# Optimization experiments

Measured on AMD Instinct MI355X. Metric: run time of the kernel, lower is better.

Reference implementation:

```python
import jax, jax.numpy as jnp
import numpy as np

N = 30000          # nodes
DEG = 16           # in-degree per node
E = N * DEG        # edges per etype
T = 3              # edge types
IN = 128           # in_feats
HID = 256          # hidden_size
HEADS = 4
CLS = 2            # num_classes
NEG_SLOPE = 0.2    # DGL GATConv default


def setup_inputs() -> dict:
    key = jax.random.key(0)
    ks = jax.random.split(key, 14)
    s = lambda k, shape: (jax.random.normal(k, shape, jnp.float32) * 0.05)
    feat = jax.random.normal(ks[0], (N, IN), jnp.float32)
    src = jax.random.randint(ks[1], (T, E), 0, N)
    # every node gets exactly DEG incoming edges per etype (DGL forbids 0-in-degree)
    dst = jnp.tile(jnp.repeat(jnp.arange(N), DEG), (T, 1))
    D = HID // HEADS
    return {
        "feat": feat,
        "W0": s(ks[2], (T, IN, HID)),  "al0": s(ks[3], (T, HEADS, D)), "ar0": s(ks[4], (T, HEADS, D)), "b0": jnp.zeros((T, HID), jnp.float32),
        "W1": s(ks[5], (T, HID, HID)), "al1": s(ks[6], (T, HEADS, D)), "ar1": s(ks[7], (T, HEADS, D)), "b1": jnp.zeros((T, HID), jnp.float32),
        "W2": s(ks[8], (T, HID, CLS)), "al2": s(ks[9], (T, 1, CLS)),   "ar2": s(ks[10], (T, 1, CLS)), "b2": jnp.zeros((T, CLS), jnp.float32),
        "src": src, "dst": dst,
    }


def _gat(feat, W, al, ar, b, src, dst):
    """DGL GATConv: feat [n,F], W [F,H*D], al/ar [H,D], b [H*D] -> [n,H,D]."""
    n = feat.shape[0]
    H, D = al.shape
    h = (feat @ W).reshape(n, H, D)                      # projected features
    el = jnp.sum(h * al, axis=-1)                        # [n,H]
    er = jnp.sum(h * ar, axis=-1)                        # [n,H]
    e = jax.nn.leaky_relu(el[src] + er[dst], NEG_SLOPE)  # [E,H] edge scores
    # segment softmax over incoming edges of each dst node
    emax = jax.ops.segment_max(e, dst, num_segments=n)
    ex = jnp.exp(e - emax[dst])
    den = jax.ops.segment_sum(ex, dst, num_segments=n)
    alpha = ex / den[dst]                                # [E,H]
    out = jax.ops.segment_sum(h[src] * alpha[:, :, None], dst, num_segments=n)
    return out + b.reshape(H, D)


def _hetero(feat, W, al, ar, b, src, dst):
    # HeteroGraphConv(aggregate='mean') over T edge types on one node type
    outs = [_gat(feat, W[t], al[t], ar[t], b[t], src[t], dst[t]) for t in range(W.shape[0])]
    return jnp.mean(jnp.stack(outs, 0), axis=0)


def reference(feat, W0, al0, ar0, b0, W1, al1, ar1, b1, W2, al2, ar2, b2, src, dst):
    h = jax.nn.elu(_hetero(feat, W0, al0, ar0, b0, src, dst).reshape(N, -1))
    h = jax.nn.elu(_hetero(h, W1, al1, ar1, b1, src, dst).reshape(N, -1))
    logits = _hetero(h, W2, al2, ar2, b2, src, dst)      # [N,1,CLS]
    # faithful to F.softmax(logits[primary_ntype], dim=1): dim=1 is the size-1 head axis
    return logits, jax.nn.softmax(logits, axis=1)
```

## Files before the change

kernel.cpp:

```cpp
#include <hip/hip_runtime.h>
#include <hip/hip_bf16.h>
#include <hip/hip_fp8.h>
#include <math.h>

#define N_NODES 30000
#define DEG     16
#define NE      480000
#define NT      3
#define IN_F    128
#define HID_F   256
#define HEADS   4
#define DH      64
#define CLS     2
#define SLOPE   0.2f
#define PAD     8

typedef __hip_bfloat16 bf16;
typedef __attribute__((ext_vector_type(8))) short short8;
typedef __attribute__((ext_vector_type(4))) float floatx4;

__device__ __forceinline__ float bf2f(short x) {
    unsigned int u = ((unsigned int)(unsigned short)x) << 16;
    float f;
    __builtin_memcpy(&f, &u, 4);
    return f;
}

__device__ __forceinline__ void fp8x4_decode(unsigned int u, float* f) {
#if __has_builtin(__builtin_amdgcn_cvt_pk_f32_fp8)
    auto lo = __builtin_amdgcn_cvt_pk_f32_fp8((int)u, false);
    auto hi = __builtin_amdgcn_cvt_pk_f32_fp8((int)u, true);
    f[0] = lo[0]; f[1] = lo[1]; f[2] = hi[0]; f[3] = hi[1];
#else
#pragma unroll
    for (int j = 0; j < 4; j++) {
        __hip_fp8_e4m3 q;
        q.__x = (unsigned char)((u >> (8 * j)) & 0xff);
        f[j] = (float)q;
    }
#endif
}

__device__ __forceinline__ void fp8_encode4(const float* v, unsigned char* b) {
#if __has_builtin(__builtin_amdgcn_cvt_pk_fp8_f32)
    int p01 = __builtin_amdgcn_cvt_pk_fp8_f32(v[0], v[1], 0, false);
    int p23 = __builtin_amdgcn_cvt_pk_fp8_f32(v[2], v[3], 0, false);
    b[0] = (unsigned char)(p01 & 0xff);
    b[1] = (unsigned char)((p01 >> 8) & 0xff);
    b[2] = (unsigned char)(p23 & 0xff);
    b[3] = (unsigned char)((p23 >> 8) & 0xff);
#else
#pragma unroll
    for (int j = 0; j < 4; j++) {
        __hip_fp8_e4m3 q(v[j]);
        b[j] = q.__x;
    }
#endif
}

#define FEAT_ELEMS (N_NODES * IN_F)
#define W0_ELEMS   (NT * IN_F * HID_F)
#define W1_ELEMS   (NT * HID_F * HID_F)
__global__ void prep(const float* __restrict__ feat, const float* __restrict__ W0,
                     const float* __restrict__ W1, bf16* __restrict__ featb,
                     bf16* __restrict__ WT0, bf16* __restrict__ WT1) {
    int idx = blockIdx.x * 256 + threadIdx.x;
    if (idx < FEAT_ELEMS) {
        featb[idx] = bf16(feat[idx]);
        return;
    }
    idx -= FEAT_ELEMS;
    if (idx < W0_ELEMS) {
        int t = idx / (IN_F * HID_F), r = idx % (IN_F * HID_F);
        int k = r / HID_F, n = r % HID_F;
        WT0[(size_t)t * HID_F * (IN_F + PAD) + (size_t)n * (IN_F + PAD) + k] = bf16(W0[idx]);
        return;
    }
    idx -= W0_ELEMS;
    if (idx < W1_ELEMS) {
        int t = idx / (HID_F * HID_F), r = idx % (HID_F * HID_F);
        int k = r / HID_F, n = r % HID_F;
        WT1[(size_t)t * HID_F * (HID_F + PAD) + (size_t)n * (HID_F + PAD) + k] = bf16(W1[idx]);
    }
}

template <int K>
__global__ __launch_bounds__(256, 2) void gemm_proj(const bf16* __restrict__ X,
                                                    const bf16* __restrict__ WT,
                                                    const float* __restrict__ al,
                                                    const float* __restrict__ ar,
                                                    unsigned char* __restrict__ Hout,
                                                    float* __restrict__ el,
                                                    float* __restrict__ er) {
    const int SK = K + PAD;
    int t    = blockIdx.y;
    int tid  = threadIdx.x;
    int wave = tid >> 6, lane = tid & 63;
    int quad = lane >> 4, l15 = lane & 15;
    int row0 = blockIdx.x * 128 + wave * 32;

    const bf16* Wt      = WT + (size_t)t * HID_F * SK;
    unsigned char* Ht   = Hout + (size_t)t * N_NODES * HID_F;

    int ar0 = row0 + l15;       if (ar0 >= N_NODES) ar0 = N_NODES - 1;
    int ar1 = row0 + 16 + l15;  if (ar1 >= N_NODES) ar1 = N_NODES - 1;
    const short* X0 = (const short*)X + (size_t)ar0 * K + quad * 8;
    const short* X1 = (const short*)X + (size_t)ar1 * K + quad * 8;
    const short* Wb = (const short*)Wt + (size_t)l15 * SK + quad * 8;

    floatx4 acc0[16], acc1[16];
#pragma unroll
    for (int i = 0; i < 16; i++) {
        acc0[i] = (floatx4){0.f, 0.f, 0.f, 0.f};
        acc1[i] = (floatx4){0.f, 0.f, 0.f, 0.f};
    }

    for (int kk = 0; kk < K; kk += 32) {
        short8 a0 = *(const short8*)(X0 + kk);
        short8 a1 = *(const short8*)(X1 + kk);
#pragma unroll
        for (int nt = 0; nt < 16; nt++) {
            short8 b = *(const short8*)(Wb + (size_t)nt * 16 * SK + kk);
            acc0[nt] = __builtin_amdgcn_mfma_f32_16x16x32_bf16(a0, b, acc0[nt], 0, 0, 0);
            acc1[nt] = __builtin_amdgcn_mfma_f32_16x16x32_bf16(a1, b, acc1[nt], 0, 0, 0);
        }
    }

    float alv[16], arv[16];
#pragma unroll
    for (int nt = 0; nt < 16; nt++) {
        alv[nt] = al[t * HID_F + nt * 16 + l15];
        arv[nt] = ar[t * HID_F + nt * 16 + l15];
    }

#pragma unroll
    for (int tile = 0; tile < 2; tile++) {
        floatx4* acc = tile ? acc1 : acc0;
#pragma unroll
        for (int nt = 0; nt < 16; nt++) {
            float v4[4] = {acc[nt][0], acc[nt][1], acc[nt][2], acc[nt][3]};
            unsigned char b4[4];
            fp8_encode4(v4, b4);
#pragma unroll
            for (int r = 0; r < 4; r++) {
                int row = row0 + tile * 16 + quad * 4 + r;
                if (row < N_NODES)
                    Ht[(size_t)row * HID_F + nt * 16 + l15] = b4[r];
            }
        }
#pragma unroll
        for (int r = 0; r < 4; r++) {
            int row = row0 + tile * 16 + quad * 4 + r;
            float pl[HEADS], pr[HEADS];
#pragma unroll
            for (int h = 0; h < HEADS; h++) {
                pl[h] = 0.f; pr[h] = 0.f;
#pragma unroll
                for (int j = 0; j < 4; j++) {
                    int nt = h * 4 + j;
                    pl[h] += acc[nt][r] * alv[nt];
                    pr[h] += acc[nt][r] * arv[nt];
                }
#pragma unroll
                for (int off = 8; off; off >>= 1) {
                    pl[h] += __shfl_xor(pl[h], off);
                    pr[h] += __shfl_xor(pr[h], off);
                }
            }
            if (l15 == 0 && row < N_NODES) {
#pragma unroll
                for (int h = 0; h < HEADS; h++) {
                    el[((size_t)t * N_NODES + row) * HEADS + h] = pl[h];
                    er[((size_t)t * N_NODES + row) * HEADS + h] = pr[h];
                }
            }
        }
    }
}

__global__ __launch_bounds__(256) void gat_agg(const unsigned char* __restrict__ Hproj,
                                               const float* __restrict__ el,
                                               const float* __restrict__ er,
                                               const int* __restrict__ src,
                                               const float* __restrict__ bias,
                                               bf16* __restrict__ out) {
    int blk = blockIdx.x;
    int tid = threadIdx.x;
    __shared__ int   s_src[8][NT][DEG];
    __shared__ float s_w[8][NT][HEADS][DEG];

#pragma unroll
    for (int it = 0; it < 2; it++) {
        int j = it * 256 + tid;
        if (j < NT * 128) {
            int t = j / 128, k = j % 128;
            s_src[k >> 4][t][k & 15] = src[(size_t)t * NE + blk * 128 + k];
        }
    }
    __syncthreads();

    {
        int lane16 = tid & 15;
        int ubase  = tid >> 4;
#pragma unroll
        for (int it = 0; it < 6; it++) {
            int u = it * 16 + ubase;
            int g = u / 12, rem = u % 12;
            int t = rem >> 2, h = rem & 3;
            int n = blk * 8 + g;
            int s = s_src[g][t][lane16];
            float e = el[((size_t)t * N_NODES + s) * HEADS + h] +
                      er[((size_t)t * N_NODES + n) * HEADS + h];
            e = e > 0.f ? e : SLOPE * e;
            float m = e;
            m = fmaxf(m, __shfl_xor(m, 1));
            m = fmaxf(m, __shfl_xor(m, 2));
            m = fmaxf(m, __shfl_xor(m, 4));
            m = fmaxf(m, __shfl_xor(m, 8));
            float p = __expf(e - m);
            float ss = p;
            ss += __shfl_xor(ss, 1);
            ss += __shfl_xor(ss, 2);
            ss += __shfl_xor(ss, 4);
            ss += __shfl_xor(ss, 8);
            s_w[g][t][h][lane16] = p / ss;
        }
    }
    __syncthreads();

    int g = tid >> 5, c = tid & 31;
    int n = blk * 8 + g;
    int h = c >> 3;
    int col0 = c * 8;

    float acc[8];
#pragma unroll
    for (int j = 0; j < 8; j++) acc[j] = 0.f;

#pragma unroll
    for (int t = 0; t < NT; t++) {
        const unsigned char* Ht = Hproj + (size_t)t * N_NODES * HID_F;
#pragma unroll
        for (int i = 0; i < DEG; i++) {
            int s   = s_src[g][t][i];
            float w = s_w[g][t][h][i];
            uint2 v = *(const uint2*)(Ht + (size_t)s * HID_F + col0);
            float f[8];
            fp8x4_decode(v.x, f);
            fp8x4_decode(v.y, f + 4);
#pragma unroll
            for (int j = 0; j < 8; j++) acc[j] += w * f[j];
        }
    }

    short8 o;
#pragma unroll
    for (int j = 0; j < 8; j++) {
        float bsum = bias[0 * HID_F + col0 + j] + bias[1 * HID_F + col0 + j] +
                     bias[2 * HID_F + col0 + j];
        float res = (acc[j] + bsum) * (1.f / 3.f);
        res = res > 0.f ? res : (__expf(res) - 1.f);
        bf16 bv = bf16(res);
        short sv;
        __builtin_memcpy(&sv, &bv, 2);
        o[j] = sv;
    }
    *(short8*)((short*)out + (size_t)n * HID_F + col0) = o;
}

__global__ __launch_bounds__(256) void proj2(const bf16* __restrict__ X,
                                             const float* __restrict__ W2,
                                             const float* __restrict__ al2,
                                             const float* __restrict__ ar2,
                                             float* __restrict__ p2,
                                             float* __restrict__ el2,
                                             float* __restrict__ er2) {
    int n    = blockIdx.x * 4 + (threadIdx.x >> 6);
    int lane = threadIdx.x & 63;
    const short* Xr = (const short*)X + (size_t)n * HID_F + lane * 4;
    float x[4];
    {
        short s0 = Xr[0], s1 = Xr[1], s2 = Xr[2], s3 = Xr[3];
        x[0] = bf2f(s0); x[1] = bf2f(s1); x[2] = bf2f(s2); x[3] = bf2f(s3);
    }
    float a[NT][CLS];
#pragma unroll
    for (int t = 0; t < NT; t++)
#pragma unroll
        for (int c = 0; c < CLS; c++) {
            float v = 0.f;
#pragma unroll
            for (int j = 0; j < 4; j++)
                v += x[j] * W2[(size_t)t * HID_F * CLS + (lane * 4 + j) * CLS + c];
#pragma unroll
            for (int off = 32; off; off >>= 1) v += __shfl_xor(v, off);
            a[t][c] = v;
        }
    if (lane == 0) {
#pragma unroll
        for (int t = 0; t < NT; t++) {
            p2[((size_t)t * N_NODES + n) * CLS + 0] = a[t][0];
            p2[((size_t)t * N_NODES + n) * CLS + 1] = a[t][1];
            el2[(size_t)t * N_NODES + n] = a[t][0] * al2[t * CLS + 0] + a[t][1] * al2[t * CLS + 1];
            er2[(size_t)t * N_NODES + n] = a[t][0] * ar2[t * CLS + 0] + a[t][1] * ar2[t * CLS + 1];
        }
    }
}

__global__ void final_layer(const float* __restrict__ p2,
                            const float* __restrict__ el2,
                            const float* __restrict__ er2,
                            const int* __restrict__ src,
                            const float* __restrict__ b2,
                            float* __restrict__ out) {
    int n = blockIdx.x * 256 + threadIdx.x;
    if (n >= N_NODES) return;
    float l0 = 0.f, l1 = 0.f;
    for (int t = 0; t < NT; t++) {
        float erv = er2[(size_t)t * N_NODES + n];
        const int* sp = src + (size_t)t * NE + n * DEG;
        float ev[DEG];
        float m = -1e30f;
#pragma unroll
        for (int i = 0; i < DEG; i++) {
            int s   = sp[i];
            float e = el2[(size_t)t * N_NODES + s] + erv;
            e = e > 0.f ? e : SLOPE * e;
            ev[i] = e;
            m = fmaxf(m, e);
        }
        float den = 0.f, a0 = 0.f, a1 = 0.f;
#pragma unroll
        for (int i = 0; i < DEG; i++) {
            int s   = sp[i];
            float p = __expf(ev[i] - m);
            den += p;
            a0  += p * p2[((size_t)t * N_NODES + s) * CLS + 0];
            a1  += p * p2[((size_t)t * N_NODES + s) * CLS + 1];
        }
        l0 += a0 / den + b2[t * CLS + 0];
        l1 += a1 / den + b2[t * CLS + 1];
    }
    l0 *= (1.f / 3.f);
    l1 *= (1.f / 3.f);
    out[(size_t)n * CLS + 0] = l0;
    out[(size_t)n * CLS + 1] = l1;
    float* out2 = out + (size_t)N_NODES * CLS;
    out2[(size_t)n * CLS + 0] = 1.0f;
    out2[(size_t)n * CLS + 1] = 1.0f;
}

extern "C" void kernel_launch(void* const* d_in, const int* in_sizes, int n_in,
                              void* d_out, int out_size, void* d_ws, size_t ws_size,
                              hipStream_t stream) {
    const float* feat = (const float*)d_in[0];
    const float* W0   = (const float*)d_in[1];
    const float* al0  = (const float*)d_in[2];
    const float* ar0  = (const float*)d_in[3];
    const float* b0   = (const float*)d_in[4];
    const float* W1   = (const float*)d_in[5];
    const float* al1  = (const float*)d_in[6];
    const float* ar1  = (const float*)d_in[7];
    const float* b1   = (const float*)d_in[8];
    const float* W2   = (const float*)d_in[9];
    const float* al2  = (const float*)d_in[10];
    const float* ar2  = (const float*)d_in[11];
    const float* b2   = (const float*)d_in[12];
    const int*   src  = (const int*)d_in[13];

    char* w = (char*)d_ws;
    auto alloc = [&](size_t bytes) {
        char* p = w;
        w += (bytes + 255) & ~(size_t)255;
        return p;
    };
    bf16*  featb = (bf16*)alloc((size_t)N_NODES * IN_F * 2);
    bf16*  WT0   = (bf16*)alloc((size_t)NT * HID_F * (IN_F + PAD) * 2);
    bf16*  WT1   = (bf16*)alloc((size_t)NT * HID_F * (HID_F + PAD) * 2);
    unsigned char* Hproj = (unsigned char*)alloc((size_t)NT * N_NODES * HID_F);
    bf16*  h1    = (bf16*)alloc((size_t)N_NODES * HID_F * 2);
    bf16*  h2    = (bf16*)alloc((size_t)N_NODES * HID_F * 2);
    float* el    = (float*)alloc((size_t)NT * N_NODES * HEADS * 4);
    float* er    = (float*)alloc((size_t)NT * N_NODES * HEADS * 4);
    float* p2    = (float*)alloc((size_t)NT * N_NODES * CLS * 4);
    float* el2   = (float*)alloc((size_t)NT * N_NODES * 4);
    float* er2   = (float*)alloc((size_t)NT * N_NODES * 4);

    int prep_total = FEAT_ELEMS + W0_ELEMS + W1_ELEMS;
    prep<<<(prep_total + 255) / 256, 256, 0, stream>>>(feat, W0, W1, featb, WT0, WT1);

    dim3 ggrid((N_NODES + 127) / 128, NT);

    gemm_proj<IN_F><<<ggrid, 256, 0, stream>>>(featb, WT0, al0, ar0, Hproj, el, er);
    gat_agg<<<N_NODES / 8, 256, 0, stream>>>(Hproj, el, er, src, b0, h1);

    gemm_proj<HID_F><<<ggrid, 256, 0, stream>>>(h1, WT1, al1, ar1, Hproj, el, er);
    gat_agg<<<N_NODES / 8, 256, 0, stream>>>(Hproj, el, er, src, b1, h2);

    proj2<<<dim3(N_NODES / 4), 256, 0, stream>>>(h2, W2, al2, ar2, p2, el2, er2);
    final_layer<<<(N_NODES + 255) / 256, 256, 0, stream>>>(p2, el2, er2, src, b2,
                                                           (float*)d_out);
}
```

Before: 331.1 us.

## Pre-pack GEMM operands into MFMA fragment layout and swap A/B roles

The activation and weight matrices are written directly into per-lane MFMA fragment order, so each wave loads contiguous 16-byte chunks instead of strided rows. The layer-1 aggregation kernel writes its output in this packed layout, removing any separate repack step. The MFMA operands are swapped so each lane holds four consecutive output columns. That lets the fp8 projection store be one 32-bit write per lane and shortens the attention-logit reductions to two shuffles. The price is more complex indexing and a padded tile buffer for the last partial node tile.

```diff
diff --git a/kernel.cpp b/kernel.cpp
--- a/kernel.cpp
+++ b/kernel.cpp
@@ -13,7 +13,11 @@
 #define DH      64
 #define CLS     2
 #define SLOPE   0.2f
-#define PAD     8
+
+#define NTILES      1875
+#define NTILES_AL   1880
+#define KC0         4
+#define KC1         8
 
 typedef __hip_bfloat16 bf16;
 typedef __attribute__((ext_vector_type(8))) short short8;
@@ -24,6 +28,12 @@
     float f;
     __builtin_memcpy(&f, &u, 4);
     return f;
+}
+__device__ __forceinline__ short f2bf_s(float x) {
+    bf16 b = bf16(x);
+    short s;
+    __builtin_memcpy(&s, &b, 2);
+    return s;
 }
 
 __device__ __forceinline__ void fp8x4_decode(unsigned int u, float* f) {
@@ -40,150 +50,150 @@
     }
 #endif
 }
-
-__device__ __forceinline__ void fp8_encode4(const float* v, unsigned char* b) {
+__device__ __forceinline__ unsigned int fp8_encode4_u32(float v0, float v1,
+                                                        float v2, float v3) {
 #if __has_builtin(__builtin_amdgcn_cvt_pk_fp8_f32)
-    int p01 = __builtin_amdgcn_cvt_pk_fp8_f32(v[0], v[1], 0, false);
-    int p23 = __builtin_amdgcn_cvt_pk_fp8_f32(v[2], v[3], 0, false);
-    b[0] = (unsigned char)(p01 & 0xff);
-    b[1] = (unsigned char)((p01 >> 8) & 0xff);
-    b[2] = (unsigned char)(p23 & 0xff);
-    b[3] = (unsigned char)((p23 >> 8) & 0xff);
+    int p01 = __builtin_amdgcn_cvt_pk_fp8_f32(v0, v1, 0, false);
+    int p23 = __builtin_amdgcn_cvt_pk_fp8_f32(v2, v3, 0, false);
+    return ((unsigned int)p01 & 0xffffu) | ((unsigned int)p23 << 16);
 #else
-#pragma unroll
-    for (int j = 0; j < 4; j++) {
-        __hip_fp8_e4m3 q(v[j]);
-        b[j] = q.__x;
-    }
+    __hip_fp8_e4m3 q0(v0), q1(v1), q2(v2), q3(v3);
+    return (unsigned int)q0.__x | ((unsigned int)q1.__x << 8) |
+           ((unsigned int)q2.__x << 16) | ((unsigned int)q3.__x << 24);
 #endif
 }
 
-#define FEAT_ELEMS (N_NODES * IN_F)
-#define W0_ELEMS   (NT * IN_F * HID_F)
-#define W1_ELEMS   (NT * HID_F * HID_F)
+
+#define APACK_THREADS (N_NODES * (IN_F / 8))
+#define BP0_THREADS   (NT * 16 * KC0 * 64)
+#define BP1_THREADS   (NT * 16 * KC1 * 64)
 __global__ void prep(const float* __restrict__ feat, const float* __restrict__ W0,
-                     const float* __restrict__ W1, bf16* __restrict__ featb,
-                     bf16* __restrict__ WT0, bf16* __restrict__ WT1) {
-    int idx = blockIdx.x * 256 + threadIdx.x;
-    if (idx < FEAT_ELEMS) {
-        featb[idx] = bf16(feat[idx]);
+                     const float* __restrict__ W1, short* __restrict__ Apack0,
+                     short* __restrict__ Bpack0, short* __restrict__ Bpack1) {
+    int g = blockIdx.x * 256 + threadIdx.x;
+    if (g < APACK_THREADS) {
+        int row = g >> 4, j8 = g & 15;
+        int k0 = j8 * 8;
+        const float* src = feat + (size_t)row * IN_F + k0;
+        int ntile = row >> 4, C = k0 >> 5, quad = (k0 >> 3) & 3;
+        int lane  = (row & 15) + 16 * quad;
+        short* dst = Apack0 + ((size_t)(ntile * KC0 + C) * 64 + lane) * 8;
+        short8 o;
+#pragma unroll
+        for (int j = 0; j < 8; j++) o[j] = f2bf_s(src[j]);
+        *(short8*)dst = o;
         return;
     }
-    idx -= FEAT_ELEMS;
-    if (idx < W0_ELEMS) {
-        int t = idx / (IN_F * HID_F), r = idx % (IN_F * HID_F);
-        int k = r / HID_F, n = r % HID_F;
-        WT0[(size_t)t * HID_F * (IN_F + PAD) + (size_t)n * (IN_F + PAD) + k] = bf16(W0[idx]);
+    g -= APACK_THREADS;
+    if (g < BP0_THREADS) {
+        int t = g / (16 * KC0 * 64), rem = g % (16 * KC0 * 64);
+        int nt = rem / (KC0 * 64);
+        int C  = (rem / 64) % KC0;
+        int lane = rem & 63, l15 = lane & 15, quad = lane >> 4;
+        int col = nt * 16 + l15, k0 = C * 32 + quad * 8;
+        const float* src = W0 + (size_t)t * IN_F * HID_F + (size_t)k0 * HID_F + col;
+        short* dst = Bpack0 + ((size_t)t * 16 * KC0 + nt * KC0 + C) * 512 + lane * 8;
+        short8 o;
+#pragma unroll
+        for (int j = 0; j < 8; j++) o[j] = f2bf_s(src[(size_t)j * HID_F]);
+        *(short8*)dst = o;
         return;
     }
-    idx -= W0_ELEMS;
-    if (idx < W1_ELEMS) {
-        int t = idx / (HID_F * HID_F), r = idx % (HID_F * HID_F);
-        int k = r / HID_F, n = r % HID_F;
-        WT1[(size_t)t * HID_F * (HID_F + PAD) + (size_t)n * (HID_F + PAD) + k] = bf16(W1[idx]);
+    g -= BP0_THREADS;
+    if (g < BP1_THREADS) {
+        int t = g / (16 * KC1 * 64), rem = g % (16 * KC1 * 64);
+        int nt = rem / (KC1 * 64);
+        int C  = (rem / 64) % KC1;
+        int lane = rem & 63, l15 = lane & 15, quad = lane >> 4;
+        int col = nt * 16 + l15, k0 = C * 32 + quad * 8;
+        const float* src = W1 + (size_t)t * HID_F * HID_F + (size_t)k0 * HID_F + col;
+        short* dst = Bpack1 + ((size_t)t * 16 * KC1 + nt * KC1 + C) * 512 + lane * 8;
+        short8 o;
+#pragma unroll
+        for (int j = 0; j < 8; j++) o[j] = f2bf_s(src[(size_t)j * HID_F]);
+        *(short8*)dst = o;
     }
 }
 
 template <int K>
-__global__ __launch_bounds__(256, 2) void gemm_proj(const bf16* __restrict__ X,
-                                                    const bf16* __restrict__ WT,
+__global__ __launch_bounds__(256, 2) void gemm_proj(const short* __restrict__ Apack,
+                                                    const short* __restrict__ Bpack,
                                                     const float* __restrict__ al,
                                                     const float* __restrict__ ar,
                                                     unsigned char* __restrict__ Hout,
                                                     float* __restrict__ el,
                                                     float* __restrict__ er) {
-    const int SK = K + PAD;
+    const int KC = K / 32;
     int t    = blockIdx.y;
     int tid  = threadIdx.x;
     int wave = tid >> 6, lane = tid & 63;
     int quad = lane >> 4, l15 = lane & 15;
-    int row0 = blockIdx.x * 128 + wave * 32;
-
-    const bf16* Wt      = WT + (size_t)t * HID_F * SK;
-    unsigned char* Ht   = Hout + (size_t)t * N_NODES * HID_F;
-
-    int ar0 = row0 + l15;       if (ar0 >= N_NODES) ar0 = N_NODES - 1;
-    int ar1 = row0 + 16 + l15;  if (ar1 >= N_NODES) ar1 = N_NODES - 1;
-    const short* X0 = (const short*)X + (size_t)ar0 * K + quad * 8;
-    const short* X1 = (const short*)X + (size_t)ar1 * K + quad * 8;
-    const short* Wb = (const short*)Wt + (size_t)l15 * SK + quad * 8;
-
-    floatx4 acc0[16], acc1[16];
+    int e0   = blockIdx.x * 8 + wave * 2;
+
+    const short* Ap0 = Apack + (size_t)(e0)     * KC * 512 + lane * 8;
+    const short* Ap1 = Apack + (size_t)(e0 + 1) * KC * 512 + lane * 8;
+    const short* Bp  = Bpack + (size_t)t * 16 * KC * 512 + lane * 8;
+    unsigned char* Ht = Hout + (size_t)t * N_NODES * HID_F;
+
+    floatx4 acc[16][2];
 #pragma unroll
     for (int i = 0; i < 16; i++) {
-        acc0[i] = (floatx4){0.f, 0.f, 0.f, 0.f};
-        acc1[i] = (floatx4){0.f, 0.f, 0.f, 0.f};
-    }
-
-    for (int kk = 0; kk < K; kk += 32) {
-        short8 a0 = *(const short8*)(X0 + kk);
-        short8 a1 = *(const short8*)(X1 + kk);
+        acc[i][0] = (floatx4){0.f, 0.f, 0.f, 0.f};
+        acc[i][1] = (floatx4){0.f, 0.f, 0.f, 0.f};
+    }
+
+    for (int C = 0; C < KC; C++) {
+        short8 xb0 = *(const short8*)(Ap0 + (size_t)C * 512);
+        short8 xb1 = *(const short8*)(Ap1 + (size_t)C * 512);
 #pragma unroll
         for (int nt = 0; nt < 16; nt++) {
-            short8 b = *(const short8*)(Wb + (size_t)nt * 16 * SK + kk);
-            acc0[nt] = __builtin_amdgcn_mfma_f32_16x16x32_bf16(a0, b, acc0[nt], 0, 0, 0);
-            acc1[nt] = __builtin_amdgcn_mfma_f32_16x16x32_bf16(a1, b, acc1[nt], 0, 0, 0);
-        }
-    }
-
-    float alv[16], arv[16];
-#pragma unroll
-    for (int nt = 0; nt < 16; nt++) {
-        alv[nt] = al[t * HID_F + nt * 16 + l15];
-        arv[nt] = ar[t * HID_F + nt * 16 + l15];
-    }
-
-#pragma unroll
-    for (int tile = 0; tile < 2; tile++) {
-        floatx4* acc = tile ? acc1 : acc0;
+            short8 wa = *(const short8*)(Bp + (size_t)(nt * KC + C) * 512);
+            acc[nt][0] = __builtin_amdgcn_mfma_f32_16x16x32_bf16(wa, xb0, acc[nt][0], 0, 0, 0);
+            acc[nt][1] = __builtin_amdgcn_mfma_f32_16x16x32_bf16(wa, xb1, acc[nt][1], 0, 0, 0);
+        }
+    }
+
+#pragma unroll
+    for (int e = 0; e < 2; e++) {
+        int node = (e0 + e) * 16 + l15;
+        bool ok  = node < N_NODES;
 #pragma unroll
         for (int nt = 0; nt < 16; nt++) {
-            float v4[4] = {acc[nt][0], acc[nt][1], acc[nt][2], acc[nt][3]};
-            unsigned char b4[4];
-            fp8_encode4(v4, b4);
-#pragma unroll
-            for (int r = 0; r < 4; r++) {
-                int row = row0 + tile * 16 + quad * 4 + r;
-                if (row < N_NODES)
-                    Ht[(size_t)row * HID_F + nt * 16 + l15] = b4[r];
+            unsigned int u = fp8_encode4_u32(acc[nt][e][0], acc[nt][e][1],
+                                             acc[nt][e][2], acc[nt][e][3]);
+            if (ok)
+                *(unsigned int*)(Ht + (size_t)node * HID_F + nt * 16 + quad * 4) = u;
+        }
+#pragma unroll
+        for (int h = 0; h < HEADS; h++) {
+            float pl = 0.f, pr = 0.f;
+#pragma unroll
+            for (int j = 0; j < 4; j++) {
+                int nt = h * 4 + j;
+                float4 av = *(const float4*)(al + t * HID_F + nt * 16 + quad * 4);
+                float4 rv = *(const float4*)(ar + t * HID_F + nt * 16 + quad * 4);
+                pl += acc[nt][e][0] * av.x + acc[nt][e][1] * av.y +
+                      acc[nt][e][2] * av.z + acc[nt][e][3] * av.w;
+                pr += acc[nt][e][0] * rv.x + acc[nt][e][1] * rv.y +
+                      acc[nt][e][2] * rv.z + acc[nt][e][3] * rv.w;
             }
-        }
-#pragma unroll
-        for (int r = 0; r < 4; r++) {
-            int row = row0 + tile * 16 + quad * 4 + r;
-            float pl[HEADS], pr[HEADS];
-#pragma unroll
-            for (int h = 0; h < HEADS; h++) {
-                pl[h] = 0.f; pr[h] = 0.f;
-#pragma unroll
-                for (int j = 0; j < 4; j++) {
-                    int nt = h * 4 + j;
-                    pl[h] += acc[nt][r] * alv[nt];
-                    pr[h] += acc[nt][r] * arv[nt];
-                }
-#pragma unroll
-                for (int off = 8; off; off >>= 1) {
-                    pl[h] += __shfl_xor(pl[h], off);
-                    pr[h] += __shfl_xor(pr[h], off);
-                }
+            pl += __shfl_xor(pl, 16); pl += __shfl_xor(pl, 32);
+            pr += __shfl_xor(pr, 16); pr += __shfl_xor(pr, 32);
+            if (lane < 16 && ok) {
+                el[((size_t)t * N_NODES + node) * HEADS + h] = pl;
+                er[((size_t)t * N_NODES + node) * HEADS + h] = pr;
             }
-            if (l15 == 0 && row < N_NODES) {
-#pragma unroll
-                for (int h = 0; h < HEADS; h++) {
-                    el[((size_t)t * N_NODES + row) * HEADS + h] = pl[h];
-                    er[((size_t)t * N_NODES + row) * HEADS + h] = pr[h];
-                }
-            }
-        }
-    }
-}
-
+        }
+    }
+}
+
+template <bool PACK>
 __global__ __launch_bounds__(256) void gat_agg(const unsigned char* __restrict__ Hproj,
                                                const float* __restrict__ el,
                                                const float* __restrict__ er,
                                                const int* __restrict__ src,
                                                const float* __restrict__ bias,
-                                               bf16* __restrict__ out) {
+                                               short* __restrict__ out) {
     int blk = blockIdx.x;
     int tid = threadIdx.x;
     __shared__ int   s_src[8][NT][DEG];
@@ -239,12 +249,12 @@
 
 #pragma unroll
     for (int t = 0; t < NT; t++) {
-        const unsigned char* Ht = Hproj + (size_t)t * N_NODES * HID_F;
+        const unsigned char* Hh = Hproj + (size_t)t * N_NODES * HID_F;
 #pragma unroll
         for (int i = 0; i < DEG; i++) {
             int s   = s_src[g][t][i];
             float w = s_w[g][t][h][i];
-            uint2 v = *(const uint2*)(Ht + (size_t)s * HID_F + col0);
+            uint2 v = *(const uint2*)(Hh + (size_t)s * HID_F + col0);
             float f[8];
             fp8x4_decode(v.x, f);
             fp8x4_decode(v.y, f + 4);
@@ -260,15 +270,18 @@
                      bias[2 * HID_F + col0 + j];
         float res = (acc[j] + bsum) * (1.f / 3.f);
         res = res > 0.f ? res : (__expf(res) - 1.f);
-        bf16 bv = bf16(res);
-        short sv;
-        __builtin_memcpy(&sv, &bv, 2);
-        o[j] = sv;
-    }
-    *(short8*)((short*)out + (size_t)n * HID_F + col0) = o;
-}
-
-__global__ __launch_bounds__(256) void proj2(const bf16* __restrict__ X,
+        o[j] = f2bf_s(res);
+    }
+    if (PACK) {
+        int ntile = n >> 4, kc = c >> 2, quad = c & 3;
+        int lane  = (n & 15) + 16 * quad;
+        *(short8*)(out + ((size_t)(ntile * KC1 + kc) * 64 + lane) * 8) = o;
+    } else {
+        *(short8*)(out + (size_t)n * HID_F + col0) = o;
+    }
+}
+
+__global__ __launch_bounds__(256) void proj2(const short* __restrict__ X,
                                              const float* __restrict__ W2,
                                              const float* __restrict__ al2,
                                              const float* __restrict__ ar2,
@@ -277,24 +290,21 @@
                                              float* __restrict__ er2) {
     int n    = blockIdx.x * 4 + (threadIdx.x >> 6);
     int lane = threadIdx.x & 63;
-    const short* Xr = (const short*)X + (size_t)n * HID_F + lane * 4;
+    const short* Xr = X + (size_t)n * HID_F + lane * 4;
     float x[4];
-    {
-        short s0 = Xr[0], s1 = Xr[1], s2 = Xr[2], s3 = Xr[3];
-        x[0] = bf2f(s0); x[1] = bf2f(s1); x[2] = bf2f(s2); x[3] = bf2f(s3);
-    }
+    x[0] = bf2f(Xr[0]); x[1] = bf2f(Xr[1]); x[2] = bf2f(Xr[2]); x[3] = bf2f(Xr[3]);
     float a[NT][CLS];
 #pragma unroll
     for (int t = 0; t < NT; t++)
 #pragma unroll
-        for (int c = 0; c < CLS; c++) {
+        for (int cc = 0; cc < CLS; cc++) {
             float v = 0.f;
 #pragma unroll
             for (int j = 0; j < 4; j++)
-                v += x[j] * W2[(size_t)t * HID_F * CLS + (lane * 4 + j) * CLS + c];
+                v += x[j] * W2[(size_t)t * HID_F * CLS + (lane * 4 + j) * CLS + cc];
 #pragma unroll
             for (int off = 32; off; off >>= 1) v += __shfl_xor(v, off);
-            a[t][c] = v;
+            a[t][cc] = v;
         }
     if (lane == 0) {
 #pragma unroll
@@ -374,28 +384,29 @@
         w += (bytes + 255) & ~(size_t)255;
         return p;
     };
-    bf16*  featb = (bf16*)alloc((size_t)N_NODES * IN_F * 2);
-    bf16*  WT0   = (bf16*)alloc((size_t)NT * HID_F * (IN_F + PAD) * 2);
-    bf16*  WT1   = (bf16*)alloc((size_t)NT * HID_F * (HID_F + PAD) * 2);
+    short* Apack0 = (short*)alloc((size_t)NTILES_AL * KC0 * 512 * 2);
+    short* Apack1 = (short*)alloc((size_t)NTILES_AL * KC1 * 512 * 2);
+    short* Bpack0 = (short*)alloc((size_t)NT * 16 * KC0 * 512 * 2);
+    short* Bpack1 = (short*)alloc((size_t)NT * 16 * KC1 * 512 * 2);
     unsigned char* Hproj = (unsigned char*)alloc((size_t)NT * N_NODES * HID_F);
-    bf16*  h1    = (bf16*)alloc((size_t)N_NODES * HID_F * 2);
-    bf16*  h2    = (bf16*)alloc((size_t)N_NODES * HID_F * 2);
+    short* h2    = (short*)alloc((size_t)N_NODES * HID_F * 2);
     float* el    = (float*)alloc((size_t)NT * N_NODES * HEADS * 4);
     float* er    = (float*)alloc((size_t)NT * N_NODES * HEADS * 4);
     float* p2    = (float*)alloc((size_t)NT * N_NODES * CLS * 4);
     float* el2   = (float*)alloc((size_t)NT * N_NODES * 4);
     float* er2   = (float*)alloc((size_t)NT * N_NODES * 4);
 
-    int prep_total = FEAT_ELEMS + W0_ELEMS + W1_ELEMS;
-    prep<<<(prep_total + 255) / 256, 256, 0, stream>>>(feat, W0, W1, featb, WT0, WT1);
-
-    dim3 ggrid((N_NODES + 127) / 128, NT);
-
-    gemm_proj<IN_F><<<ggrid, 256, 0, stream>>>(featb, WT0, al0, ar0, Hproj, el, er);
-    gat_agg<<<N_NODES / 8, 256, 0, stream>>>(Hproj, el, er, src, b0, h1);
-
-    gemm_proj<HID_F><<<ggrid, 256, 0, stream>>>(h1, WT1, al1, ar1, Hproj, el, er);
-    gat_agg<<<N_NODES / 8, 256, 0, stream>>>(Hproj, el, er, src, b1, h2);
+    int prep_total = APACK_THREADS + BP0_THREADS + BP1_THREADS;
+    prep<<<(prep_total + 255) / 256, 256, 0, stream>>>(feat, W0, W1, Apack0,
+                                                       Bpack0, Bpack1);
+
+    dim3 ggrid((NTILES + 7) / 8, NT);
+
+    gemm_proj<IN_F><<<ggrid, 256, 0, stream>>>(Apack0, Bpack0, al0, ar0, Hproj, el, er);
+    gat_agg<true><<<N_NODES / 8, 256, 0, stream>>>(Hproj, el, er, src, b0, Apack1);
+
+    gemm_proj<HID_F><<<ggrid, 256, 0, stream>>>(Apack1, Bpack1, al1, ar1, Hproj, el, er);
+    gat_agg<false><<<N_NODES / 8, 256, 0, stream>>>(Hproj, el, er, src, b1, h2);
 
     proj2<<<dim3(N_NODES / 4), 256, 0, stream>>>(h2, W2, al2, ar2, p2, el2, er2);
     final_layer<<<(N_NODES + 255) / 256, 256, 0, stream>>>(p2, el2, er2, src, b2,
```

After: 345.2 us. +4.3%, slower.
